# Optimization experiments

Hardware: AMD Instinct MI355X
Metric: run time of the kernel (lower is better)

Reference implementation:

```python
import jax, jax.numpy as jnp
import numpy as np
from jax import lax

B, T, IN_DIM, HIDDEN = 8, 4096, 1024, 1024


def setup_inputs() -> dict:
    key = jax.random.key(0)
    k_x, k_wd, k_wb = jax.random.split(key, 3)
    x = jax.random.normal(k_x, (B, T, IN_DIM), dtype=jnp.float32)
    h0 = jnp.zeros((B, HIDDEN), dtype=jnp.float32)
    # nn.Linear default init ~ U(-1/sqrt(in), 1/sqrt(in)); b_proj.weight ~ N(0, 0.02)
    lim = 1.0 / np.sqrt(IN_DIM)
    Wd = jax.random.uniform(k_wd, (HIDDEN, IN_DIM), jnp.float32, -lim, lim)
    bd = jnp.zeros((HIDDEN,), dtype=jnp.float32)
    Wb = 0.02 * jax.random.normal(k_wb, (HIDDEN, IN_DIM), dtype=jnp.float32)
    bb = jnp.zeros((HIDDEN,), dtype=jnp.float32)
    # 'hasani' init: A_log = log(linspace(0.5, 2.0, hidden))
    A_log = jnp.log(jnp.linspace(0.5, 2.0, HIDDEN, dtype=jnp.float32))
    return {"x": x, "h0": h0, "Wd": Wd, "bd": bd, "Wb": Wb, "bb": bb, "A_log": A_log}


def _combine(c1, c2):
    # composition of affine maps h -> a*h + b
    a1, b1 = c1
    a2, b2 = c2
    return a1 * a2, a2 * b1 + b2


def reference(x, h0, Wd, bd, Wb, bb, A_log):
    # projections: (B,T,in) @ (in,hidden)
    delta = jax.nn.softplus(jnp.einsum('bti,hi->bth', x, Wd) + bd)
    b_t = delta * (jnp.einsum('bti,hi->bth', x, Wb) + bb)
    A = jnp.exp(A_log)                      # (H,) decay rate
    A_t = jnp.exp(-delta * A)               # (B,T,H)
    # parallel (Blelloch/Heinsen-style) associative scan over T:
    # cumulative affine maps give h_t = A_cum_t * h0 + B_cum_t
    A_cum, B_cum = lax.associative_scan(_combine, (A_t, b_t), axis=1)
    h_full = A_cum * h0[:, None, :] + B_cum  # (B,T,H)
    return jnp.tanh(h_full)                  # bound=True
```

## Files before the change

kernel.cpp:

```cpp
#include <hip/hip_runtime.h>
#include <math.h>

#define B_DIM 8
#define T_DIM 4096
#define K_DIM 1024
#define H_DIM 1024
#define M_DIM (B_DIM * T_DIM)

#define CH 64
#define NC (T_DIM / CH)
#define BK 64
#define NKS (K_DIM / BK)

typedef short bf16x8 __attribute__((ext_vector_type(8)));
typedef float f32x4  __attribute__((ext_vector_type(4)));

__device__ __forceinline__ unsigned short f2bf(float f) {
  unsigned int u = __builtin_bit_cast(unsigned int, f);
  u += 0x7FFFu + ((u >> 16) & 1u);
  return (unsigned short)(u >> 16);
}

__device__ __forceinline__ void gload_lds16(const void* g, void* l) {
  __builtin_amdgcn_global_load_lds(
      (const __attribute__((address_space(1))) unsigned int*)g,
      (__attribute__((address_space(3))) unsigned int*)l,
      16 , 0 , 0 );
}

__device__ __forceinline__ float softplus_fast(float x) {
  float e = __expf(-fabsf(x));
  return fmaxf(x, 0.f) + __logf(1.f + e);
}

__device__ __forceinline__ float tanh_fast(float x) {
  float e = __expf(2.f * x);
  return 1.f - 2.f * __builtin_amdgcn_rcpf(e + 1.f);
}

__global__ __launch_bounds__(256) void k_cvt(const float* __restrict__ in,
                                             unsigned short* __restrict__ out,
                                             int n8) {
  int i = blockIdx.x * 256 + threadIdx.x;
  if (i >= n8) return;
  float4 v0 = ((const float4*)in)[i * 2 + 0];
  float4 v1 = ((const float4*)in)[i * 2 + 1];
  bf16x8 r;
  r[0] = (short)f2bf(v0.x); r[1] = (short)f2bf(v0.y);
  r[2] = (short)f2bf(v0.z); r[3] = (short)f2bf(v0.w);
  r[4] = (short)f2bf(v1.x); r[5] = (short)f2bf(v1.y);
  r[6] = (short)f2bf(v1.z); r[7] = (short)f2bf(v1.w);
  ((bf16x8*)out)[i] = r;
}

#define MFMA_Q(AF, BF, MQ, NQ)                                                 \
  do {                                                                         \
    __builtin_amdgcn_s_setprio(1);                                             \
    _Pragma("unroll")                                                          \
    for (int mm = 0; mm < 4; mm++)                                             \
      _Pragma("unroll")                                                        \
      for (int nn = 0; nn < 2; nn++)                                           \
        _Pragma("unroll")                                                      \
        for (int kk = 0; kk < 2; kk++)                                         \
          acc[(MQ)*4 + mm][(NQ)*2 + nn] =                                      \
              __builtin_amdgcn_mfma_f32_16x16x32_bf16(                         \
                  AF[mm*2 + kk], BF[nn*2 + kk],                                \
                  acc[(MQ)*4 + mm][(NQ)*2 + nn], 0, 0, 0);                     \
    __builtin_amdgcn_s_setprio(0);                                             \
  } while (0)

__global__ __launch_bounds__(512, 2) void k_gemm_dual(
    const unsigned short* __restrict__ Xb,
    const unsigned short* __restrict__ Wdb,
    const unsigned short* __restrict__ Wbb,
    const float* __restrict__ bd,
    const float* __restrict__ bb,
    const float* __restrict__ A_log,
    float* __restrict__ a_out,
    float* __restrict__ b_out,
    float* __restrict__ aggA,
    float* __restrict__ aggB)
{
  __shared__ unsigned short As[2][256 * BK];
  __shared__ unsigned short Bs[2][256 * BK];

  const int tid  = threadIdx.x;
  const int wgid = blockIdx.x;
  const int xcd  = wgid & 7;
  const int j    = wgid >> 3;
  const int bm   = (xcd * 16 + (j >> 3)) * 256;
  const int bn   = (j & 7) * 128;

  const int w    = tid >> 6;
  const int lane = tid & 63;
  const int wm   = (w >> 2) * 128;
  const int wq   = w & 3;
  const int wn   = wq * 64;

  f32x4 acc[8][4];
  const f32x4 z4 = {0.f, 0.f, 0.f, 0.f};
#pragma unroll
  for (int m = 0; m < 8; m++)
#pragma unroll
    for (int n = 0; n < 4; n++) acc[m][n] = z4;

  const int fr = lane & 15;
  const int hi = lane >> 4;

  const unsigned short* gA[4];
  const unsigned short* gB[4];
  int ldsoff[4];
#pragma unroll
  for (int jj = 0; jj < 4; jj++) {
    int idx = jj * 512 + tid;
    int row = idx >> 3;
    int cg  = (idx & 7) ^ (row & 7);
    ldsoff[jj] = idx * 16;
    gA[jj] = Xb + (size_t)(bm + row) * K_DIM + (size_t)(cg * 8);
    int h = bn + (row >> 6) * 32 + (row & 31);
    const unsigned short* Wsrc = (row & 32) ? Wbb : Wdb;
    gB[jj] = Wsrc + (size_t)h * K_DIM + (size_t)(cg * 8);
  }

#define STAGE(T, D)                                                           \
  do {                                                                        \
    _Pragma("unroll")                                                         \
    for (int jj = 0; jj < 4; jj++) {                                          \
      gload_lds16(gA[jj] + (T) * BK, (char*)As[D] + ldsoff[jj]);              \
      gload_lds16(gB[jj] + (T) * BK, (char*)Bs[D] + ldsoff[jj]);              \
    }                                                                         \
  } while (0)

  const int ch0 = hi ^ (fr & 7);
  const int ch1 = ch0 ^ 4;
  const char* bA0 = (const char*)As + (size_t)((wm + fr) * 128 + ch0 * 16);
  const char* bA1 = (const char*)As + (size_t)((wm + fr) * 128 + ch1 * 16);
  const char* bB0 = (const char*)Bs + (size_t)((wn + fr) * 128 + ch0 * 16);
  const char* bB1 = (const char*)Bs + (size_t)((wn + fr) * 128 + ch1 * 16);

#define RDA(DST, D, MQ)                                                       \
  _Pragma("unroll")                                                           \
  for (int mm = 0; mm < 4; mm++) {                                            \
    DST[mm*2+0] = *(const bf16x8*)(bA0 + (D)*32768 + ((MQ)*64 + mm*16)*128);  \
    DST[mm*2+1] = *(const bf16x8*)(bA1 + (D)*32768 + ((MQ)*64 + mm*16)*128);  \
  }
#define RDB(DST, D, NQ)                                                       \
  _Pragma("unroll")                                                           \
  for (int nn = 0; nn < 2; nn++) {                                            \
    DST[nn*2+0] = *(const bf16x8*)(bB0 + (D)*32768 + ((NQ)*32 + nn*16)*128);  \
    DST[nn*2+1] = *(const bf16x8*)(bB1 + (D)*32768 + ((NQ)*32 + nn*16)*128);  \
  }

#define TILE(T, D, NXT)                                                       \
  do {                                                                        \
    if (NXT) STAGE((T) + 1, (D) ^ 1);                                         \
    bf16x8 A0[8], A1[8], B0[4], B1[4];                                        \
    RDA(A0, D, 0); RDB(B0, D, 0);                                             \
    MFMA_Q(A0, B0, 0, 0);                                                     \
    RDB(B1, D, 1);                                                            \
    MFMA_Q(A0, B1, 0, 1);                                                     \
    RDA(A1, D, 1);                                                            \
    MFMA_Q(A1, B0, 1, 0);                                                     \
    MFMA_Q(A1, B1, 1, 1);                                                     \
    if (NXT) {                                                                \
      asm volatile("s_waitcnt vmcnt(0)" ::: "memory");                        \
      __builtin_amdgcn_s_barrier();                                           \
    }                                                                         \
  } while (0)

  STAGE(0, 0);
  asm volatile("s_waitcnt vmcnt(0)" ::: "memory");
  __builtin_amdgcn_s_barrier();

#pragma unroll 1
  for (int t = 0; t < NKS; t += 2) {
    TILE(t,     0, true);
    TILE(t + 1, 1, (t + 2) < NKS);
  }

  const int col   = fr;
  const int rbase = hi * 4;
  const int bidx  = bm >> 12;
  const int cch0  = ((bm + wm) & (T_DIM - 1)) >> 6;

#pragma unroll
  for (int np = 0; np < 2; np++) {
    int gn = bn + wq * 32 + np * 16 + col;
    float bdv = bd[gn];
    float bbv = bb[gn];
    float Ah  = __expf(A_log[gn]);
    float segA[8], segB[8];
#pragma unroll
    for (int m = 0; m < 8; m++) {
      float sA = 1.f, sB = 0.f;
#pragma unroll
      for (int r = 0; r < 4; r++) {
        int gm = bm + wm + m * 16 + rbase + r;
        float z1  = acc[m][np][r] + bdv;
        float z2  = acc[m][np + 2][r] + bbv;
        float dlt = softplus_fast(z1);
        float av  = __expf(-dlt * Ah);
        float bv  = dlt * z2;
        size_t off = (size_t)gm * H_DIM + (size_t)gn;
        a_out[off] = av;
        b_out[off] = bv;
        sB = fmaf(av, sB, bv);
        sA *= av;
      }
      segA[m] = sA; segB[m] = sB;
    }
#pragma unroll
    for (int g = 0; g < 2; g++) {
      float chA = 1.f, chB = 0.f;
#pragma unroll
      for (int mi = 0; mi < 4; mi++) {
        int m = g * 4 + mi;
#pragma unroll
        for (int h2 = 0; h2 < 4; h2++) {
          float sa = __shfl(segA[m], col + h2 * 16, 64);
          float sb = __shfl(segB[m], col + h2 * 16, 64);
          chB = fmaf(sa, chB, sb);
          chA *= sa;
        }
      }
      if (lane < 16) {
        size_t o = ((size_t)(bidx * NC + cch0 + g) << 10) + (size_t)gn;
        aggA[o] = chA;
        aggB[o] = chB;
      }
    }
  }
}

__global__ __launch_bounds__(256) void k_scan_chunks(
    const float* __restrict__ aggA, const float* __restrict__ aggB,
    const float* __restrict__ h0, float* __restrict__ hstart)
{
  int idx = blockIdx.x * 256 + threadIdx.x;
  int h   = idx & (H_DIM - 1);
  int b   = idx >> 10;
  float hc = h0[idx];
  for (int c = 0; c < NC; c++) {
    size_t o = ((size_t)(b * NC + c) << 10) + (size_t)h;
    hstart[o] = hc;
    hc = fmaf(aggA[o], hc, aggB[o]);
  }
}

__global__ __launch_bounds__(256) void k_scan_apply(
    const float* __restrict__ a_arr, const float* b_arr,
    const float* __restrict__ hstart, float* out)
{
  int idx = blockIdx.x * 256 + threadIdx.x;
  int h   = idx & (H_DIM - 1);
  int bc  = idx >> 10;
  int c   = bc & (NC - 1);
  int b   = bc >> 6;
  size_t base = ((size_t)b * T_DIM + (size_t)c * CH) * H_DIM + (size_t)h;
  float hc = hstart[idx];
#pragma unroll 4
  for (int i = 0; i < CH; i++) {
    size_t o = base + (size_t)i * H_DIM;
    float at = a_arr[o];
    float bt = b_arr[o];
    hc = fmaf(at, hc, bt);
    out[o] = tanh_fast(hc);
  }
}

extern "C" void kernel_launch(void* const* d_in, const int* in_sizes, int n_in,
                              void* d_out, int out_size, void* d_ws, size_t ws_size,
                              hipStream_t stream) {
  const float* x     = (const float*)d_in[0];
  const float* h0    = (const float*)d_in[1];
  const float* Wd    = (const float*)d_in[2];
  const float* bd    = (const float*)d_in[3];
  const float* Wb    = (const float*)d_in[4];
  const float* bb    = (const float*)d_in[5];
  const float* A_log = (const float*)d_in[6];
  float* out = (float*)d_out;

  char* ws = (char*)d_ws;
  unsigned short* xb   = (unsigned short*)(ws + 0);
  unsigned short* wdb  = (unsigned short*)(ws + 67108864);
  unsigned short* wbb  = (unsigned short*)(ws + 69206016);
  float*          aarr = (float*)(ws + 71303168);
  float*          aggA = (float*)(ws + 205520896);
  float*          aggB = (float*)(ws + 207618048);
  float*          hst  = (float*)(ws + 209715200);
  float*          barr = out;

  k_cvt<<<(M_DIM * K_DIM / 8) / 256, 256, 0, stream>>>(x, xb, M_DIM * K_DIM / 8);
  k_cvt<<<(H_DIM * K_DIM / 8) / 256, 256, 0, stream>>>(Wd, wdb, H_DIM * K_DIM / 8);
  k_cvt<<<(H_DIM * K_DIM / 8) / 256, 256, 0, stream>>>(Wb, wbb, H_DIM * K_DIM / 8);

  k_gemm_dual<<<(M_DIM / 256) * (H_DIM / 128), 512, 0, stream>>>(
      xb, wdb, wbb, bd, bb, A_log, aarr, barr, aggA, aggB);

  k_scan_chunks<<<(B_DIM * H_DIM) / 256,      256, 0, stream>>>(aggA, aggB, h0, hst);
  k_scan_apply <<<(B_DIM * NC * H_DIM) / 256, 256, 0, stream>>>(aarr, barr, hst, out);
}
```

Before: 336.1 us.

## Use BK=32 with 4-stage LDS ring and prefetch distance two in dual GEMM

Halves the K tile to 32 and replaces the double-buffered LDS scheme with a 4-slot ring, issuing global->LDS loads two tiles ahead and waiting with a partial vmcnt instead of draining all loads before each barrier. This hides more global-load latency behind MFMA work. It drops the XOR swizzle on LDS rows, which may bring bank conflicts on the 64-byte row reads, and changes launch bounds to one block per CU, lowering occupancy. The barrier per K-step also doubles in count.

```diff
diff --git a/kernel.cpp b/kernel.cpp
--- a/kernel.cpp
+++ b/kernel.cpp
@@ -9,7 +9,7 @@
 
 #define CH 64
 #define NC (T_DIM / CH)
-#define BK 64
+#define BK 32
 #define NKS (K_DIM / BK)
 
 typedef short bf16x8 __attribute__((ext_vector_type(8)));
@@ -53,23 +53,7 @@
   ((bf16x8*)out)[i] = r;
 }
 
-#define MFMA_Q(AF, BF, MQ, NQ)                                                 \
-  do {                                                                         \
-    __builtin_amdgcn_s_setprio(1);                                             \
-    _Pragma("unroll")                                                          \
-    for (int mm = 0; mm < 4; mm++)                                             \
-      _Pragma("unroll")                                                        \
-      for (int nn = 0; nn < 2; nn++)                                           \
-        _Pragma("unroll")                                                      \
-        for (int kk = 0; kk < 2; kk++)                                         \
-          acc[(MQ)*4 + mm][(NQ)*2 + nn] =                                      \
-              __builtin_amdgcn_mfma_f32_16x16x32_bf16(                         \
-                  AF[mm*2 + kk], BF[nn*2 + kk],                                \
-                  acc[(MQ)*4 + mm][(NQ)*2 + nn], 0, 0, 0);                     \
-    __builtin_amdgcn_s_setprio(0);                                             \
-  } while (0)
-
-__global__ __launch_bounds__(512, 2) void k_gemm_dual(
+__global__ __launch_bounds__(512, 1) void k_gemm_dual(
     const unsigned short* __restrict__ Xb,
     const unsigned short* __restrict__ Wdb,
     const unsigned short* __restrict__ Wbb,
@@ -81,8 +65,8 @@
     float* __restrict__ aggA,
     float* __restrict__ aggB)
 {
-  __shared__ unsigned short As[2][256 * BK];
-  __shared__ unsigned short Bs[2][256 * BK];
+  __shared__ unsigned short As[4][256 * BK];
+  __shared__ unsigned short Bs[4][256 * BK];
 
   const int tid  = threadIdx.x;
   const int wgid = blockIdx.x;
@@ -107,75 +91,65 @@
   const int fr = lane & 15;
   const int hi = lane >> 4;
 
-  const unsigned short* gA[4];
-  const unsigned short* gB[4];
-  int ldsoff[4];
-#pragma unroll
-  for (int jj = 0; jj < 4; jj++) {
+  const unsigned short* gA[2];
+  const unsigned short* gB[2];
+  int ldsoff[2];
+#pragma unroll
+  for (int jj = 0; jj < 2; jj++) {
     int idx = jj * 512 + tid;
-    int row = idx >> 3;
-    int cg  = (idx & 7) ^ (row & 7);
+    int row = idx >> 2;
+    int ch  = idx & 3;
     ldsoff[jj] = idx * 16;
-    gA[jj] = Xb + (size_t)(bm + row) * K_DIM + (size_t)(cg * 8);
+    gA[jj] = Xb + (((size_t)(bm + row)) << 10) + (size_t)(ch * 8);
     int h = bn + (row >> 6) * 32 + (row & 31);
     const unsigned short* Wsrc = (row & 32) ? Wbb : Wdb;
-    gB[jj] = Wsrc + (size_t)h * K_DIM + (size_t)(cg * 8);
+    gB[jj] = Wsrc + (((size_t)h) << 10) + (size_t)(ch * 8);
   }
 
 #define STAGE(T, D)                                                           \
   do {                                                                        \
     _Pragma("unroll")                                                         \
-    for (int jj = 0; jj < 4; jj++) {                                          \
+    for (int jj = 0; jj < 2; jj++) {                                          \
       gload_lds16(gA[jj] + (T) * BK, (char*)As[D] + ldsoff[jj]);              \
       gload_lds16(gB[jj] + (T) * BK, (char*)Bs[D] + ldsoff[jj]);              \
     }                                                                         \
   } while (0)
 
-  const int ch0 = hi ^ (fr & 7);
-  const int ch1 = ch0 ^ 4;
-  const char* bA0 = (const char*)As + (size_t)((wm + fr) * 128 + ch0 * 16);
-  const char* bA1 = (const char*)As + (size_t)((wm + fr) * 128 + ch1 * 16);
-  const char* bB0 = (const char*)Bs + (size_t)((wn + fr) * 128 + ch0 * 16);
-  const char* bB1 = (const char*)Bs + (size_t)((wn + fr) * 128 + ch1 * 16);
-
-#define RDA(DST, D, MQ)                                                       \
-  _Pragma("unroll")                                                           \
-  for (int mm = 0; mm < 4; mm++) {                                            \
-    DST[mm*2+0] = *(const bf16x8*)(bA0 + (D)*32768 + ((MQ)*64 + mm*16)*128);  \
-    DST[mm*2+1] = *(const bf16x8*)(bA1 + (D)*32768 + ((MQ)*64 + mm*16)*128);  \
-  }
-#define RDB(DST, D, NQ)                                                       \
-  _Pragma("unroll")                                                           \
-  for (int nn = 0; nn < 2; nn++) {                                            \
-    DST[nn*2+0] = *(const bf16x8*)(bB0 + (D)*32768 + ((NQ)*32 + nn*16)*128);  \
-    DST[nn*2+1] = *(const bf16x8*)(bB1 + (D)*32768 + ((NQ)*32 + nn*16)*128);  \
-  }
-
-#define TILE(T, D, NXT)                                                       \
+  const char* bA = (const char*)As + ((wm + fr) * 64 + hi * 16);
+  const char* bB = (const char*)Bs + ((wn + fr) * 64 + hi * 16);
+
+#define BODY(T, D)                                                            \
   do {                                                                        \
-    if (NXT) STAGE((T) + 1, (D) ^ 1);                                         \
-    bf16x8 A0[8], A1[8], B0[4], B1[4];                                        \
-    RDA(A0, D, 0); RDB(B0, D, 0);                                             \
-    MFMA_Q(A0, B0, 0, 0);                                                     \
-    RDB(B1, D, 1);                                                            \
-    MFMA_Q(A0, B1, 0, 1);                                                     \
-    RDA(A1, D, 1);                                                            \
-    MFMA_Q(A1, B0, 1, 0);                                                     \
-    MFMA_Q(A1, B1, 1, 1);                                                     \
-    if (NXT) {                                                                \
-      asm volatile("s_waitcnt vmcnt(0)" ::: "memory");                        \
-      __builtin_amdgcn_s_barrier();                                           \
-    }                                                                         \
+    if ((T) + 2 < NKS) asm volatile("s_waitcnt vmcnt(4)" ::: "memory");       \
+    else               asm volatile("s_waitcnt vmcnt(0)" ::: "memory");       \
+    __builtin_amdgcn_s_barrier();                                             \
+    if ((T) + 2 < NKS) STAGE((T) + 2, ((D) + 2) & 3);                         \
+    bf16x8 Af[8], Bf[4];                                                      \
+    _Pragma("unroll")                                                         \
+    for (int m = 0; m < 8; m++)                                               \
+      Af[m] = *(const bf16x8*)(bA + (D) * 16384 + m * 1024);                  \
+    _Pragma("unroll")                                                         \
+    for (int n = 0; n < 4; n++)                                               \
+      Bf[n] = *(const bf16x8*)(bB + (D) * 16384 + n * 1024);                  \
+    __builtin_amdgcn_s_setprio(1);                                            \
+    _Pragma("unroll")                                                         \
+    for (int m = 0; m < 8; m++)                                               \
+      _Pragma("unroll")                                                       \
+      for (int n = 0; n < 4; n++)                                             \
+        acc[m][n] = __builtin_amdgcn_mfma_f32_16x16x32_bf16(                  \
+            Af[m], Bf[n], acc[m][n], 0, 0, 0);                                \
+    __builtin_amdgcn_s_setprio(0);                                            \
   } while (0)
 
   STAGE(0, 0);
-  asm volatile("s_waitcnt vmcnt(0)" ::: "memory");
-  __builtin_amdgcn_s_barrier();
+  STAGE(1, 1);
 
 #pragma unroll 1
-  for (int t = 0; t < NKS; t += 2) {
-    TILE(t,     0, true);
-    TILE(t + 1, 1, (t + 2) < NKS);
+  for (int tb = 0; tb < NKS; tb += 4) {
+    BODY(tb + 0, 0);
+    BODY(tb + 1, 1);
+    BODY(tb + 2, 2);
+    BODY(tb + 3, 3);
   }
 
   const int col   = fr;
@@ -230,6 +204,8 @@
       }
     }
   }
+#undef BODY
+#undef STAGE
 }
 
 __global__ __launch_bounds__(256) void k_scan_chunks(
```

Result: slower. 351.3 us (+4.5%).
